# Kernel tuning notes

Measured on AMD Instinct MI355X. Metric: run time of the kernel, lower is better.

Reference implementation:

```python
import jax, jax.numpy as jnp
import numpy as np

B, T, V, E, H, DE = 64, 52, 10000, 512, 512, 2048


def _lstm_cell(x, h, c, w_ih, w_hh, b_ih, b_hh):
    # torch.nn.LSTMCell gate order: i, f, g, o
    gates = x @ w_ih.T + h @ w_hh.T + b_ih + b_hh
    i, f, g, o = jnp.split(gates, 4, axis=-1)
    c2 = jax.nn.sigmoid(f) * c + jax.nn.sigmoid(i) * jnp.tanh(g)
    h2 = jax.nn.sigmoid(o) * jnp.tanh(c2)
    return h2, c2


def _run_dir(emb_seq, img, lens, p1, p2, fc_w, fc_b):
    # emb_seq: [B, Td, E]; img: [B, H]; lens: [B] sorted descending.
    # The torch loop slices h[:batch_size_t]; since lens is sorted descending,
    # that is equivalent to masking updates where t >= (len-1). Rows that fall
    # out of the active prefix are never read again, and their predictions stay 0.
    Bd, Td = emb_seq.shape[0], emb_seq.shape[1]
    Hd = img.shape[1]
    mask = jnp.arange(Td)[None, :] < (lens - 1)[:, None]  # [B, Td]
    z = jnp.zeros((Bd, Hd), emb_seq.dtype)

    def step(carry, xs):
        h, c, h1, c1 = carry
        x, m = xs
        m2 = m[:, None]
        hn, cn = _lstm_cell(x, h, c, *p1)
        h1n, c1n = _lstm_cell(jnp.concatenate([hn, img], axis=1), h1, c1, *p2)
        carry = (jnp.where(m2, hn, h), jnp.where(m2, cn, c),
                 jnp.where(m2, h1n, h1), jnp.where(m2, c1n, c1))
        preds = jnp.where(m2, h1n @ fc_w.T + fc_b, 0.0)  # [B, V]
        return carry, preds

    _, preds = jax.lax.scan(step, (z, z, z, z), (emb_seq.transpose(1, 0, 2), mask.T))
    return preds.transpose(1, 0, 2)  # [B, Td, V]


def setup_inputs():
    key = jax.random.key(0)
    ks = iter(jax.random.split(key, 48))

    def u(shape, a=-0.1, b=0.1):
        return jax.random.uniform(next(ks), shape, minval=a, maxval=b, dtype=jnp.float32)

    inp = {}
    inp['encoder_out'] = jax.random.normal(next(ks), (B, DE), dtype=jnp.float32)
    inp['encoded_captions'] = jax.random.randint(next(ks), (B, T), 0, V)
    cl = jax.random.randint(next(ks), (B, 1), 2, T + 1)
    inp['caption_lengths'] = cl.at[0, 0].set(T)  # ensure max decode length = T-1
    # embeddings (uniform -0.1..0.1 per init_weights)
    inp['emb_w'] = u((V, E))
    inp['emb_r_w'] = u((V, E))
    # LSTM cells: torch default init uniform(-1/sqrt(H), 1/sqrt(H))
    kH = 1.0 / np.sqrt(H)
    for name, din in [('1', E), ('2', 2 * H), ('r1', E), ('r2', 2 * H)]:
        inp['w_ih' + name] = u((4 * H, din), -kH, kH)
        inp['w_hh' + name] = u((4 * H, H), -kH, kH)
        inp['b_ih' + name] = u((4 * H,), -kH, kH)
        inp['b_hh' + name] = u((4 * H,), -kH, kH)
    kD = 1.0 / np.sqrt(DE)
    inp['img_f_w'] = u((H, DE), -kD, kD)
    inp['img_f_b'] = u((H,), -kD, kD)
    inp['img_b_w'] = u((H, DE), -kD, kD)
    inp['img_b_b'] = u((H,), -kD, kD)
    inp['fc_w'] = u((V, H))
    inp['fc_b'] = jnp.zeros((V,), jnp.float32)
    inp['fcr_w'] = u((V, H))
    inp['fcr_b'] = jnp.zeros((V,), jnp.float32)
    return inp


def reference(encoder_out, encoded_captions, caption_lengths, emb_w, emb_r_w,
              w_ih1, w_hh1, b_ih1, b_hh1, w_ih2, w_hh2, b_ih2, b_hh2,
              w_ihr1, w_hhr1, b_ihr1, b_hhr1, w_ihr2, w_hhr2, b_ihr2, b_hhr2,
              img_f_w, img_f_b, img_b_w, img_b_b, fc_w, fc_b, fcr_w, fcr_b):
    lens = caption_lengths[:, 0]
    order = jnp.argsort(-lens)  # descending, stable (jax argsort is stable)
    lens = lens[order]
    enc = encoder_out[order]
    caps = encoded_captions[order]
    Tc = caps.shape[1]
    # per-row reversal of the first len tokens; rest zero (matches torch loop)
    j = jnp.arange(Tc)[None, :]
    valid = j < lens[:, None]
    rev_idx = jnp.where(valid, lens[:, None] - 1 - j, 0)
    caps_rev = jnp.where(valid, jnp.take_along_axis(caps, rev_idx, axis=1), 0)
    emb = emb_w[caps]          # [B, T, E]
    emb_r = emb_r_w[caps_rev]  # [B, T, E]
    img_f = enc @ img_f_w.T + img_f_b
    img_r = enc @ img_b_w.T + img_b_b
    Td = Tc - 1  # max(decode_lengths); setup guarantees max(lens) == T
    preds = _run_dir(emb[:, :Td], img_f, lens,
                     (w_ih1, w_hh1, b_ih1, b_hh1), (w_ih2, w_hh2, b_ih2, b_hh2), fc_w, fc_b)
    preds_r = _run_dir(emb_r[:, :Td], img_r, lens,
                       (w_ihr1, w_hhr1, b_ihr1, b_hhr1), (w_ihr2, w_hhr2, b_ihr2, b_hhr2), fcr_w, fcr_b)
    return preds, preds_r, caps, caps_rev, lens - 1, order
```

## Files before the change

### kernel.cpp

```cpp
#include <hip/hip_runtime.h>
#include <stdint.h>

#define B64   64
#define T52   52
#define TD    51
#define V10K  10000
#define MP    3328
#define MR    3264
#define NPFC  10112

typedef float  f32x4  __attribute__((ext_vector_type(4)));
typedef __bf16 bf16x8 __attribute__((ext_vector_type(8)));
typedef unsigned int u32x4 __attribute__((ext_vector_type(4)));
typedef unsigned short ushort_t;

__device__ inline unsigned short f2bf(float f) {
  unsigned u = __builtin_bit_cast(unsigned, f);
  u += 0x7fffu + ((u >> 16) & 1u);
  return (unsigned short)(u >> 16);
}
__device__ inline unsigned pack2(float a, float b) {
  return (unsigned)f2bf(a) | ((unsigned)f2bf(b) << 16);
}
__device__ inline float sigm(float x) { return 1.f / (1.f + expf(-x)); }

__device__ inline void store2_sc(ushort_t* p, unsigned v) {
  asm volatile("global_store_short %0, %1, off sc1" :: "v"(p), "v"(v) : "memory");
}
__device__ inline void loadA16(const ushort_t* a, u32x4 (&h)[16]) {
  asm volatile(
    "global_load_dwordx4 %0,  %16, off sc1\n\t"
    "global_load_dwordx4 %1,  %16, off offset:64 sc1\n\t"
    "global_load_dwordx4 %2,  %16, off offset:128 sc1\n\t"
    "global_load_dwordx4 %3,  %16, off offset:192 sc1\n\t"
    "global_load_dwordx4 %4,  %16, off offset:256 sc1\n\t"
    "global_load_dwordx4 %5,  %16, off offset:320 sc1\n\t"
    "global_load_dwordx4 %6,  %16, off offset:384 sc1\n\t"
    "global_load_dwordx4 %7,  %16, off offset:448 sc1\n\t"
    "global_load_dwordx4 %8,  %16, off offset:512 sc1\n\t"
    "global_load_dwordx4 %9,  %16, off offset:576 sc1\n\t"
    "global_load_dwordx4 %10, %16, off offset:640 sc1\n\t"
    "global_load_dwordx4 %11, %16, off offset:704 sc1\n\t"
    "global_load_dwordx4 %12, %16, off offset:768 sc1\n\t"
    "global_load_dwordx4 %13, %16, off offset:832 sc1\n\t"
    "global_load_dwordx4 %14, %16, off offset:896 sc1\n\t"
    "global_load_dwordx4 %15, %16, off offset:960 sc1\n\t"
    "s_waitcnt vmcnt(0)"
    : "=&v"(h[0]),"=&v"(h[1]),"=&v"(h[2]),"=&v"(h[3]),
      "=&v"(h[4]),"=&v"(h[5]),"=&v"(h[6]),"=&v"(h[7]),
      "=&v"(h[8]),"=&v"(h[9]),"=&v"(h[10]),"=&v"(h[11]),
      "=&v"(h[12]),"=&v"(h[13]),"=&v"(h[14]),"=&v"(h[15])
    : "v"(a) : "memory");
}
__device__ inline void loadA32(const ushort_t* a, const ushort_t* b,
                               u32x4 (&ha)[16], u32x4 (&hb)[16]) {
  asm volatile(
    "global_load_dwordx4 %0,  %32, off sc1\n\t"
    "global_load_dwordx4 %1,  %32, off offset:64 sc1\n\t"
    "global_load_dwordx4 %2,  %32, off offset:128 sc1\n\t"
    "global_load_dwordx4 %3,  %32, off offset:192 sc1\n\t"
    "global_load_dwordx4 %4,  %32, off offset:256 sc1\n\t"
    "global_load_dwordx4 %5,  %32, off offset:320 sc1\n\t"
    "global_load_dwordx4 %6,  %32, off offset:384 sc1\n\t"
    "global_load_dwordx4 %7,  %32, off offset:448 sc1\n\t"
    "global_load_dwordx4 %8,  %32, off offset:512 sc1\n\t"
    "global_load_dwordx4 %9,  %32, off offset:576 sc1\n\t"
    "global_load_dwordx4 %10, %32, off offset:640 sc1\n\t"
    "global_load_dwordx4 %11, %32, off offset:704 sc1\n\t"
    "global_load_dwordx4 %12, %32, off offset:768 sc1\n\t"
    "global_load_dwordx4 %13, %32, off offset:832 sc1\n\t"
    "global_load_dwordx4 %14, %32, off offset:896 sc1\n\t"
    "global_load_dwordx4 %15, %32, off offset:960 sc1\n\t"
    "global_load_dwordx4 %16, %33, off sc1\n\t"
    "global_load_dwordx4 %17, %33, off offset:64 sc1\n\t"
    "global_load_dwordx4 %18, %33, off offset:128 sc1\n\t"
    "global_load_dwordx4 %19, %33, off offset:192 sc1\n\t"
    "global_load_dwordx4 %20, %33, off offset:256 sc1\n\t"
    "global_load_dwordx4 %21, %33, off offset:320 sc1\n\t"
    "global_load_dwordx4 %22, %33, off offset:384 sc1\n\t"
    "global_load_dwordx4 %23, %33, off offset:448 sc1\n\t"
    "global_load_dwordx4 %24, %33, off offset:512 sc1\n\t"
    "global_load_dwordx4 %25, %33, off offset:576 sc1\n\t"
    "global_load_dwordx4 %26, %33, off offset:640 sc1\n\t"
    "global_load_dwordx4 %27, %33, off offset:704 sc1\n\t"
    "global_load_dwordx4 %28, %33, off offset:768 sc1\n\t"
    "global_load_dwordx4 %29, %33, off offset:832 sc1\n\t"
    "global_load_dwordx4 %30, %33, off offset:896 sc1\n\t"
    "global_load_dwordx4 %31, %33, off offset:960 sc1\n\t"
    "s_waitcnt vmcnt(0)"
    : "=&v"(ha[0]),"=&v"(ha[1]),"=&v"(ha[2]),"=&v"(ha[3]),
      "=&v"(ha[4]),"=&v"(ha[5]),"=&v"(ha[6]),"=&v"(ha[7]),
      "=&v"(ha[8]),"=&v"(ha[9]),"=&v"(ha[10]),"=&v"(ha[11]),
      "=&v"(ha[12]),"=&v"(ha[13]),"=&v"(ha[14]),"=&v"(ha[15]),
      "=&v"(hb[0]),"=&v"(hb[1]),"=&v"(hb[2]),"=&v"(hb[3]),
      "=&v"(hb[4]),"=&v"(hb[5]),"=&v"(hb[6]),"=&v"(hb[7]),
      "=&v"(hb[8]),"=&v"(hb[9]),"=&v"(hb[10]),"=&v"(hb[11]),
      "=&v"(hb[12]),"=&v"(hb[13]),"=&v"(hb[14]),"=&v"(hb[15])
    : "v"(a), "v"(b) : "memory");
}

__global__ void k_prep(const int* __restrict__ cl, const int* __restrict__ caps,
                       float* __restrict__ out_caps, float* __restrict__ out_capr,
                       float* __restrict__ out_lm1, float* __restrict__ out_ord,
                       int* __restrict__ order_i, int* __restrict__ lensm1_i,
                       int* __restrict__ nvtab, int* __restrict__ capsS,
                       int* __restrict__ capsRev)
{
  __shared__ int L[64], O[64], Ls_s[64];
  int i = threadIdx.x;
  L[i] = cl[i];
  __syncthreads();
  if (i == 0) {
    for (int a = 0; a < 64; ++a) O[a] = a;
    for (int a = 1; a < 64; ++a) {
      int key = O[a], kl = L[key], b = a - 1;
      while (b >= 0 && L[O[b]] < kl) { O[b + 1] = O[b]; --b; }
      O[b + 1] = key;
    }
  }
  __syncthreads();
  int src = O[i];
  int Ls  = L[src];
  Ls_s[i] = Ls;
  order_i[i]  = src;
  lensm1_i[i] = Ls - 1;
  out_lm1[i]  = (float)(Ls - 1);
  out_ord[i]  = (float)src;
  int rowLocal[T52];
  for (int t = 0; t < T52; ++t) {
    int c = caps[src * T52 + t];
    rowLocal[t] = c;
    capsS[i * T52 + t]    = c;
    out_caps[i * T52 + t] = (float)c;
  }
  for (int j = 0; j < T52; ++j) {
    int rv = (j < Ls) ? rowLocal[Ls - 1 - j] : 0;
    capsRev[i * T52 + j]  = rv;
    out_capr[i * T52 + j] = (float)rv;
  }
  __syncthreads();
  if (i < TD) {
    int nv = 0;
    for (int r = 0; r < 64; ++r) nv += (Ls_s[r] - 1 > i) ? 1 : 0;
    nvtab[i] = nv;
  }
}

__global__ void k_convert(const float* __restrict__ w_ih1, const float* __restrict__ w_ihr1,
                          const float* __restrict__ fc_w, const float* __restrict__ fcr_w,
                          const float* __restrict__ b_ih1, const float* __restrict__ b_hh1,
                          const float* __restrict__ b_ihr1, const float* __restrict__ b_hhr1,
                          const float* __restrict__ w_hh1, const float* __restrict__ w_hhr1,
                          const float* __restrict__ w_ih2, const float* __restrict__ w_ihr2,
                          const float* __restrict__ w_hh2, const float* __restrict__ w_hhr2,
                          const float* __restrict__ img_f_w, const float* __restrict__ img_b_w,
                          const float* __restrict__ b_ih2, const float* __restrict__ b_hh2,
                          const float* __restrict__ b_ihr2, const float* __restrict__ b_hhr2,
                          const float* __restrict__ enc, const int* __restrict__ order_i,
                          ushort_t* __restrict__ wih1bf, ushort_t* __restrict__ fcwbf,
                          ushort_t* __restrict__ whh1bf, ushort_t* __restrict__ wih2Lbf,
                          ushort_t* __restrict__ whh2bf, ushort_t* __restrict__ wih2Ibf,
                          ushort_t* __restrict__ imgwbf, ushort_t* __restrict__ encbf,
                          float* __restrict__ biasg1, float* __restrict__ biasg2)
{
  long long gid = (long long)blockIdx.x * blockDim.x + threadIdx.x;
  const long long C1 = 2048LL * 512 / 8;
  const long long CF = (long long)NPFC * 512 / 8;
  const long long bs  = 2 * C1 + 2 * CF;
  const long long bs2 = bs + 6 * C1;
  const long long bs3 = bs2 + 2 * C1;
  const long long bs4 = bs3 + 2 * C1;
  const long long bs5 = bs4 + 32768;
  if (gid < 2 * C1) {
    int dir = gid >= C1; long long cid = gid - (long long)dir * C1;
    const float* s = (dir ? w_ihr1 : w_ih1) + cid * 8;
    ushort_t* d = wih1bf + (long long)dir * 2048 * 512 + cid * 8;
    uint4 v;
    v.x = pack2(s[0], s[1]); v.y = pack2(s[2], s[3]);
    v.z = pack2(s[4], s[5]); v.w = pack2(s[6], s[7]);
    *(uint4*)d = v;
  } else if (gid < bs) {
    long long g2 = gid - 2 * C1; int dir = g2 >= CF;
    long long cid = g2 - (long long)dir * CF;
    long long row = cid >> 6; int k8 = (int)(cid & 63) * 8;
    ushort_t* d = fcwbf + (long long)dir * NPFC * 512 + row * 512 + k8;
    uint4 v;
    if (row < V10K) {
      const float* s = (dir ? fcr_w : fc_w) + row * 512 + k8;
      v.x = pack2(s[0], s[1]); v.y = pack2(s[2], s[3]);
      v.z = pack2(s[4], s[5]); v.w = pack2(s[6], s[7]);
    } else { v.x = v.y = v.z = v.w = 0u; }
    *(uint4*)d = v;
  } else if (gid < bs2) {
    long long e = gid - bs;
    int arr = (int)(e / (2 * C1));
    long long d2 = e - (long long)arr * 2 * C1;
    int dir = d2 >= C1;
    long long cid = d2 - (long long)dir * C1;
    long long row = cid >> 6; int k8 = (int)(cid & 63) * 8;
    const float* s;
    ushort_t* d;
    if (arr == 0)      { s = (dir ? w_hhr1 : w_hh1) + row * 512  + k8; d = whh1bf; }
    else if (arr == 1) { s = (dir ? w_ihr2 : w_ih2) + row * 1024 + k8; d = wih2Lbf; }
    else               { s = (dir ? w_hhr2 : w_hh2) + row * 512  + k8; d = whh2bf; }
    d += (long long)dir * 2048 * 512 + cid * 8;
    uint4 v;
    v.x = pack2(s[0], s[1]); v.y = pack2(s[2], s[3]);
    v.z = pack2(s[4], s[5]); v.w = pack2(s[6], s[7]);
    *(uint4*)d = v;
  } else if (gid < bs3) {
    long long e = gid - bs2; int dir = e >= C1;
    long long cid = e - (long long)dir * C1;
    long long row = cid >> 6; int k8 = (int)(cid & 63) * 8;
    const float* s = (dir ? w_ihr2 : w_ih2) + row * 1024 + 512 + k8;
    ushort_t* d = wih2Ibf + (long long)dir * 2048 * 512 + cid * 8;
    uint4 v;
    v.x = pack2(s[0], s[1]); v.y = pack2(s[2], s[3]);
    v.z = pack2(s[4], s[5]); v.w = pack2(s[6], s[7]);
    *(uint4*)d = v;
  } else if (gid < bs4) {
    long long e = gid - bs3; int dir = e >= C1;
    long long cid = e - (long long)dir * C1;
    long long row = cid >> 8; int c8 = (int)(cid & 255) * 8;
    const float* s = (dir ? img_b_w : img_f_w) + row * 2048 + c8;
    ushort_t* d = imgwbf + (long long)dir * 512 * 2048 + cid * 8;
    uint4 v;
    v.x = pack2(s[0], s[1]); v.y = pack2(s[2], s[3]);
    v.z = pack2(s[4], s[5]); v.w = pack2(s[6], s[7]);
    *(uint4*)d = v;
  } else if (gid < bs5) {
    long long cid = gid - bs4;
    int m = (int)(cid >> 8); int c8 = (int)(cid & 255) * 8;
    const float* s = enc + (long long)order_i[m & 63] * 2048 + c8;
    ushort_t* d = encbf + cid * 8;
    uint4 v;
    v.x = pack2(s[0], s[1]); v.y = pack2(s[2], s[3]);
    v.z = pack2(s[4], s[5]); v.w = pack2(s[6], s[7]);
    *(uint4*)d = v;
  } else {
    long long g3 = gid - bs5;
    if (g3 < 4096) {
      int dir = g3 >= 2048; int j = (int)(g3 & 2047);
      biasg1[dir * 2048 + j] = dir ? (b_ihr1[j] + b_hhr1[j]) : (b_ih1[j] + b_hh1[j]);
    } else if (g3 < 8192) {
      long long g4 = g3 - 4096;
      int dir = g4 >= 2048; int j = (int)(g4 & 2047);
      biasg2[dir * 2048 + j] = dir ? (b_ihr2[j] + b_hhr2[j]) : (b_ih2[j] + b_hh2[j]);
    }
  }
}

__global__ void k_gather(const float* __restrict__ emb_w, const float* __restrict__ emb_r_w,
                         const int* __restrict__ capsS, const int* __restrict__ capsRev,
                         ushort_t* __restrict__ embA)
{
  long long gid = (long long)blockIdx.x * 256 + threadIdx.x;
  const long long CPD = (long long)MP * 512 / 8;
  if (gid >= 2 * CPD) return;
  int dir = gid >= CPD; long long cid = gid - (long long)dir * CPD;
  int m = (int)(cid >> 6); int k8 = (int)(cid & 63) * 8;
  ushort_t* d = embA + (long long)dir * MP * 512 + (long long)m * 512 + k8;
  uint4 v;
  if (m < MR) {
    int b = m / TD, t = m - b * TD;
    int row = dir ? capsRev[b * T52 + t] : capsS[b * T52 + t];
    const float* s = (dir ? emb_r_w : emb_w) + (long long)row * 512 + k8;
    v.x = pack2(s[0], s[1]); v.y = pack2(s[2], s[3]);
    v.z = pack2(s[4], s[5]); v.w = pack2(s[6], s[7]);
  } else { v.x = v.y = v.z = v.w = 0u; }
  *(uint4*)d = v;
}

template<int MODE>
__global__ __launch_bounds__(256)
void k_gemm(const ushort_t* __restrict__ A0, long long As,
            const ushort_t* __restrict__ B0, long long Bs,
            const float* __restrict__ bias0, const float* __restrict__ bias1,
            void* __restrict__ out0, long long Os,
            const int* __restrict__ lensm1, int Nreal, int K)
{
  __shared__ ushort_t Ab[128 * 32];
  __shared__ ushort_t Bb[128 * 32];
  int dirz = blockIdx.z;
  const ushort_t* A = A0 + dirz * As;
  const ushort_t* Bm = B0 + dirz * Bs;
  const float* bias = dirz ? bias1 : bias0;
  int tid = threadIdx.x;
  int lane = tid & 63, wid = tid >> 6;
  int wr = wid >> 1, wc = wid & 1;
  long long tm = (long long)blockIdx.x * 128, tn = (long long)blockIdx.y * 128;
  f32x4 acc[4][4] = {};
  int c0 = tid, c1 = tid + 256;
  const ushort_t* Ag0 = A + (tm + (c0 >> 2)) * K + (c0 & 3) * 8;
  const ushort_t* Ag1 = A + (tm + (c1 >> 2)) * K + (c1 & 3) * 8;
  const ushort_t* Bg0 = Bm + (tn + (c0 >> 2)) * K + (c0 & 3) * 8;
  const ushort_t* Bg1 = Bm + (tn + (c1 >> 2)) * K + (c1 & 3) * 8;
  int KK = K >> 5;
  for (int kk = 0; kk < KK; ++kk) {
    uint4 va0 = *(const uint4*)(Ag0 + kk * 32);
    uint4 va1 = *(const uint4*)(Ag1 + kk * 32);
    uint4 vb0 = *(const uint4*)(Bg0 + kk * 32);
    uint4 vb1 = *(const uint4*)(Bg1 + kk * 32);
    __syncthreads();
    *(uint4*)&Ab[c0 * 8] = va0;
    *(uint4*)&Ab[c1 * 8] = va1;
    *(uint4*)&Bb[c0 * 8] = vb0;
    *(uint4*)&Bb[c1 * 8] = vb1;
    __syncthreads();
    int koff = (lane >> 4) * 8;
    bf16x8 av[4], bv[4];
    #pragma unroll
    for (int mi = 0; mi < 4; ++mi)
      av[mi] = *(const bf16x8*)&Ab[(wr * 64 + mi * 16 + (lane & 15)) * 32 + koff];
    #pragma unroll
    for (int ni = 0; ni < 4; ++ni)
      bv[ni] = *(const bf16x8*)&Bb[(wc * 64 + ni * 16 + (lane & 15)) * 32 + koff];
    #pragma unroll
    for (int mi = 0; mi < 4; ++mi)
      #pragma unroll
      for (int ni = 0; ni < 4; ++ni)
        acc[mi][ni] = __builtin_amdgcn_mfma_f32_16x16x32_bf16(av[mi], bv[ni], acc[mi][ni], 0, 0, 0);
  }
  #pragma unroll
  for (int mi = 0; mi < 4; ++mi) {
    #pragma unroll
    for (int rr = 0; rr < 4; ++rr) {
      long long m = tm + wr * 64 + mi * 16 + ((lane >> 4) * 4) + rr;
      if (MODE == 0) {
        float* orow = (float*)out0 + dirz * Os + m * (long long)Nreal;
        #pragma unroll
        for (int ni = 0; ni < 4; ++ni) {
          int n = (int)tn + wc * 64 + ni * 16 + (lane & 15);
          orow[n] = acc[mi][ni][rr] + bias[n];
        }
      } else if (MODE == 1) {
        if (m < MR) {
          int bb = (int)(m / TD); int tt = (int)(m - (long long)bb * TD);
          bool valid = tt < lensm1[bb];
          float* orow = (float*)out0 + dirz * Os + m * (long long)Nreal;
          #pragma unroll
          for (int ni = 0; ni < 4; ++ni) {
            int n = (int)tn + wc * 64 + ni * 16 + (lane & 15);
            if (n < Nreal) orow[n] = valid ? (acc[mi][ni][rr] + bias[n]) : 0.f;
          }
        }
      } else if (MODE == 2) {
        float bm = bias[m];
        float* orow = (float*)out0 + dirz * Os + m * (long long)Nreal;
        #pragma unroll
        for (int ni = 0; ni < 4; ++ni) {
          int n = (int)tn + wc * 64 + ni * 16 + (lane & 15);
          if (n < Nreal) orow[n] = acc[mi][ni][rr] + bm;
        }
      } else {
        ushort_t* orow = (ushort_t*)out0 + dirz * Os + m * (long long)Nreal;
        #pragma unroll
        for (int ni = 0; ni < 4; ++ni) {
          int n = (int)tn + wc * 64 + ni * 16 + (lane & 15);
          orow[n] = f2bf(acc[mi][ni][rr] + bias[n]);
        }
      }
    }
  }
}

__global__ __launch_bounds__(256)
void k_txg(const float* __restrict__ xg1, float* __restrict__ xg1T)
{
  int t = blockIdx.x, jt = blockIdx.y, dir = blockIdx.z;
  __shared__ float LT[64][65];
  const float* src = xg1 + (long long)dir * MP * 2048;
  int jj = threadIdx.x & 63, br = threadIdx.x >> 6;
  for (int q = 0; q < 16; ++q) {
    int b = br * 16 + q;
    LT[b][jj] = src[((long long)b * TD + t) * 2048 + jt * 64 + jj];
  }
  __syncthreads();
  float* dst = xg1T + (((long long)dir * TD + t) * 2048 + (long long)jt * 64) * 64;
  int j = threadIdx.x >> 2, seg = threadIdx.x & 3;
  for (int q = 0; q < 4; ++q) {
    int b0 = seg * 16 + q * 4;
    float4 v = { LT[b0][j], LT[b0 + 1][j], LT[b0 + 2][j], LT[b0 + 3][j] };
    *(float4*)(dst + (long long)j * 64 + b0) = v;
  }
}

__global__ __launch_bounds__(256, 1)
void k_rec(const ushort_t* __restrict__ whh1bf, const ushort_t* __restrict__ wih2Lbf,
           const ushort_t* __restrict__ whh2bf, const float* __restrict__ xg1T,
           const float* __restrict__ xg2imgT,
           ushort_t* __restrict__ h1hist,
           ushort_t* __restrict__ h2buf,
           ushort_t* __restrict__ h2allbf, const int* __restrict__ nvtab,
           int* __restrict__ slots)
{
  const int bid = blockIdx.x;
  const bool isL2 = bid >= 64;
  int dir, ht, half;
  if (!isL2) { dir = bid >> 5; ht = bid & 31; half = 0; }
  else { int idx = bid - 64; dir = idx >> 6; int sub = idx & 63; half = sub >> 5; ht = sub & 31; }
  const int tid = threadIdx.x;
  const int lane = tid & 63, mt = tid >> 6;
  const int l15 = lane & 15, l4 = lane >> 4;
  const int jl = ht * 16 + l15;

  __shared__ ushort_t Wl[32768];
  __shared__ ushort_t Wi[32768];
  __shared__ int nv_s[64];

  {
    const ushort_t* src = (isL2 ? whh2bf : whh1bf) + (long long)dir * 2048 * 512;
    #pragma unroll
    for (int i = 0; i < 16; ++i) {
      int c = tid + i * 256;
      int nl = c >> 6;
      int kb = (c & 63) * 16;
      int row = (nl >> 4) * 512 + ht * 16 + (nl & 15);
      u32x4 v = *(const u32x4*)(src + (long long)row * 512 + (long long)(c & 63) * 8);
      *(u32x4*)((char*)Wl + nl * 1024 + (kb ^ ((nl & 7) << 4))) = v;
    }
    if (isL2) {
      const ushort_t* src2 = wih2Lbf + (long long)dir * 2048 * 512;
      #pragma unroll
      for (int i = 0; i < 16; ++i) {
        int c = tid + i * 256;
        int nl = c >> 6;
        int kb = (c & 63) * 16;
        int row = (nl >> 4) * 512 + ht * 16 + (nl & 15);
        u32x4 v = *(const u32x4*)(src2 + (long long)row * 512 + (long long)(c & 63) * 8);
        *(u32x4*)((char*)Wi + nl * 1024 + (kb ^ ((nl & 7) << 4))) = v;
      }
    }
    if (tid < TD) nv_s[tid] = nvtab[tid];
  }
  __syncthreads();

  int* aS = slots + dir * 32;
  int* bS = slots + 64 + dir * 64;

  if (!isL2) {
    const int r0 = mt * 16 + l4 * 4;
    f32x4 creg = {0.f, 0.f, 0.f, 0.f};
    for (int t = 0; t < TD; ++t) {
      bool act = (mt * 16 < nv_s[t]);
      f32x4 xv[4];
      if (act) {
        const float* xg = xg1T + ((long long)dir * TD + t) * (2048 * 64);
        #pragma unroll
        for (int g = 0; g < 4; ++g)
          xv[g] = *(const f32x4*)(xg + (long long)(g * 512 + jl) * 64 + r0);
      }
      if (t > 0) {
        if (mt == 0) {
          for (;;) {
            int v = __hip_atomic_load(&aS[lane & 31], __ATOMIC_RELAXED, __HIP_MEMORY_SCOPE_AGENT);
            if (__all(v >= t)) break;
          }
        }
        __syncthreads();
      }
      if (act) {
        const ushort_t* hsrc = h1hist + ((long long)t * 2 + dir) * (64 * 512);
        u32x4 hv[16];
        loadA16(hsrc + (long long)(mt * 16 + l15) * 512 + l4 * 8, hv);
        f32x4 acc[4] = {};
        #pragma unroll
        for (int kk = 0; kk < 16; ++kk) {
          bf16x8 av = __builtin_bit_cast(bf16x8, hv[kk]);
          int kb = kk * 64 + l4 * 16;
          #pragma unroll
          for (int g = 0; g < 4; ++g) {
            bf16x8 bv = *(const bf16x8*)((const char*)Wl + (g * 16 + l15) * 1024 + (kb ^ ((l15 & 7) << 4)));
            acc[g] = __builtin_amdgcn_mfma_f32_16x16x32_bf16(av, bv, acc[g], 0, 0, 0);
          }
        }
        ushort_t* hdst = h1hist + ((long long)(t + 1) * 2 + dir) * (64 * 512);
        f32x4 cn;
        #pragma unroll
        for (int rr = 0; rr < 4; ++rr) {
          float gi = acc[0][rr] + xv[0][rr];
          float gf = acc[1][rr] + xv[1][rr];
          float gg = acc[2][rr] + xv[2][rr];
          float go = acc[3][rr] + xv[3][rr];
          float c = sigm(gf) * creg[rr] + sigm(gi) * tanhf(gg);
          float h = sigm(go) * tanhf(c);
          cn[rr] = c;
          store2_sc(hdst + (long long)(r0 + rr) * 512 + jl, (unsigned)f2bf(h));
        }
        creg = cn;
      }
      __syncthreads();
      if (tid == 0)
        __hip_atomic_store(&aS[ht], t + 1, __ATOMIC_RELAXED, __HIP_MEMORY_SCOPE_AGENT);
    }
  } else {
    const int r0 = half * 32 + mt * 16 + l4 * 4;
    f32x4 xv2[4];
    {
      const float* xg = xg2imgT + (long long)dir * (2048 * 64);
      #pragma unroll
      for (int g = 0; g < 4; ++g)
        xv2[g] = *(const f32x4*)(xg + (long long)(g * 512 + jl) * 64 + (half * 32 + (mt & 1) * 16 + l4 * 4));
    }
    f32x4 creg = {0.f, 0.f, 0.f, 0.f};
    for (int t = 0; t < TD; ++t) {
      if (mt == 0) {
        for (;;) {
          int va = __hip_atomic_load(&aS[lane & 31], __ATOMIC_RELAXED, __HIP_MEMORY_SCOPE_AGENT);
          int vb = __hip_atomic_load(&bS[lane], __ATOMIC_RELAXED, __HIP_MEMORY_SCOPE_AGENT);
          if (__all((va >= t + 1) & (vb >= t))) break;
        }
      }
      __syncthreads();
      int nv = nv_s[t];
      if (mt < 2 && half * 32 + mt * 16 < nv) {
        const ushort_t* h1s = h1hist + ((long long)(t + 1) * 2 + dir) * (64 * 512);
        const ushort_t* h2s = h2buf + ((long long)((t + 1) & 1) * 2 + dir) * (64 * 512);
        u32x4 ha[16], hb[16];
        loadA32(h1s + (long long)(half * 32 + mt * 16 + l15) * 512 + l4 * 8,
                h2s + (long long)(half * 32 + mt * 16 + l15) * 512 + l4 * 8, ha, hb);
        f32x4 acc[4] = {};
        #pragma unroll
        for (int kk = 0; kk < 16; ++kk) {
          bf16x8 av = __builtin_bit_cast(bf16x8, ha[kk]);
          int kb = kk * 64 + l4 * 16;
          #pragma unroll
          for (int g = 0; g < 4; ++g) {
            bf16x8 bv = *(const bf16x8*)((const char*)Wi + (g * 16 + l15) * 1024 + (kb ^ ((l15 & 7) << 4)));
            acc[g] = __builtin_amdgcn_mfma_f32_16x16x32_bf16(av, bv, acc[g], 0, 0, 0);
          }
        }
        #pragma unroll
        for (int kk = 0; kk < 16; ++kk) {
          bf16x8 av = __builtin_bit_cast(bf16x8, hb[kk]);
          int kb = kk * 64 + l4 * 16;
          #pragma unroll
          for (int g = 0; g < 4; ++g) {
            bf16x8 bv = *(const bf16x8*)((const char*)Wl + (g * 16 + l15) * 1024 + (kb ^ ((l15 & 7) << 4)));
            acc[g] = __builtin_amdgcn_mfma_f32_16x16x32_bf16(av, bv, acc[g], 0, 0, 0);
          }
        }
        ushort_t* h2n = h2buf + ((long long)(t & 1) * 2 + dir) * (64 * 512);
        ushort_t* h2a = h2allbf + (long long)dir * MP * 512;
        f32x4 cn;
        #pragma unroll
        for (int rr = 0; rr < 4; ++rr) {
          float gi = acc[0][rr] + xv2[0][rr];
          float gf = acc[1][rr] + xv2[1][rr];
          float gg = acc[2][rr] + xv2[2][rr];
          float go = acc[3][rr] + xv2[3][rr];
          float c = sigm(gf) * creg[rr] + sigm(gi) * tanhf(gg);
          float h = sigm(go) * tanhf(c);
          cn[rr] = c;
          ushort_t hbb = f2bf(h);
          store2_sc(h2n + (long long)(r0 + rr) * 512 + jl, (unsigned)hbb);
          if (r0 + rr < nv)
            h2a[((long long)(r0 + rr) * TD + t) * 512 + jl] = hbb;
        }
        creg = cn;
      }
      __syncthreads();
      if (tid == 0)
        __hip_atomic_store(&bS[half * 32 + ht], t + 1, __ATOMIC_RELAXED, __HIP_MEMORY_SCOPE_AGENT);
    }
  }
}

extern "C" void kernel_launch(void* const* d_in, const int* in_sizes, int n_in,
                              void* d_out, int out_size, void* d_ws, size_t ws_size,
                              hipStream_t stream)
{
  const float* enc     = (const float*)d_in[0];
  const int*   caps    = (const int*)d_in[1];
  const int*   cl      = (const int*)d_in[2];
  const float* emb_w   = (const float*)d_in[3];
  const float* emb_r_w = (const float*)d_in[4];
  const float* w_ih1   = (const float*)d_in[5];
  const float* w_hh1   = (const float*)d_in[6];
  const float* b_ih1   = (const float*)d_in[7];
  const float* b_hh1   = (const float*)d_in[8];
  const float* w_ih2   = (const float*)d_in[9];
  const float* w_hh2   = (const float*)d_in[10];
  const float* b_ih2   = (const float*)d_in[11];
  const float* b_hh2   = (const float*)d_in[12];
  const float* w_ihr1  = (const float*)d_in[13];
  const float* w_hhr1  = (const float*)d_in[14];
  const float* b_ihr1  = (const float*)d_in[15];
  const float* b_hhr1  = (const float*)d_in[16];
  const float* w_ihr2  = (const float*)d_in[17];
  const float* w_hhr2  = (const float*)d_in[18];
  const float* b_ihr2  = (const float*)d_in[19];
  const float* b_hhr2  = (const float*)d_in[20];
  const float* img_f_w = (const float*)d_in[21];
  const float* img_f_b = (const float*)d_in[22];
  const float* img_b_w = (const float*)d_in[23];
  const float* img_b_b = (const float*)d_in[24];
  const float* fc_w    = (const float*)d_in[25];
  const float* fc_b    = (const float*)d_in[26];
  const float* fcr_w   = (const float*)d_in[27];
  const float* fcr_b   = (const float*)d_in[28];

  float* outF = (float*)d_out;
  const long long PRED = (long long)MR * V10K;
  float* o_caps = outF + 2 * PRED;
  float* o_capr = o_caps + B64 * T52;
  float* o_lm1  = o_capr + B64 * T52;
  float* o_ord  = o_lm1 + B64;
  float*    xg1       = outF;
  float*    xg1T      = outF + 14000000;
  ushort_t* whh1bf    = (ushort_t*)(outF + 27500000);
  ushort_t* wih2Lbf   = (ushort_t*)(outF + 28600000);
  ushort_t* whh2bf    = (ushort_t*)(outF + 29700000);
  ushort_t* h1hist    = (ushort_t*)(outF + 31000000);
  ushort_t* wih2Ibf   = (ushort_t*)(outF + 34600000);
  ushort_t* imgwbf    = (ushort_t*)(outF + 35700000);
  ushort_t* encbf     = (ushort_t*)(outF + 36800000);
  ushort_t* imgbf     = (ushort_t*)(outF + 37000000);

  char* w = (char*)d_ws;
  auto alloc = [&](size_t bytes) -> char* {
    char* p = w; w += (bytes + 255) & ~(size_t)255; return p;
  };
  int*      order_i  = (int*)alloc(64 * 4);
  int*      lensm1_i = (int*)alloc(64 * 4);
  int*      nvtab    = (int*)alloc(64 * 4);
  int*      capsS    = (int*)alloc(B64 * T52 * 4);
  int*      capsRev  = (int*)alloc(B64 * T52 * 4);
  float*    biasg1   = (float*)alloc(2 * 2048 * 4);
  float*    biasg2   = (float*)alloc(2 * 2048 * 4);
  float*    xg2imgT  = (float*)alloc((size_t)2 * 2048 * 64 * 4);
  char*     stateBase = alloc(262144 + 1024);
  ushort_t* h2buf = (ushort_t*)stateBase;
  int*      slotp = (int*)(stateBase + 262144);
  ushort_t* embA    = (ushort_t*)alloc((size_t)2 * MP * 512 * 2);
  ushort_t* wih1bf  = (ushort_t*)alloc((size_t)2 * 2048 * 512 * 2);
  ushort_t* fcwbf   = (ushort_t*)alloc((size_t)2 * NPFC * 512 * 2);
  ushort_t* h2allbf = (ushort_t*)alloc((size_t)2 * MP * 512 * 2);

  hipMemsetAsync(stateBase, 0, 262144 + 1024, stream);
  hipMemsetAsync(h1hist, 0, 131072, stream);

  k_prep<<<1, 64, 0, stream>>>(cl, caps, o_caps, o_capr, o_lm1, o_ord,
                               order_i, lensm1_i, nvtab, capsS, capsRev);
  k_convert<<<11360, 256, 0, stream>>>(w_ih1, w_ihr1, fc_w, fcr_w,
                                       b_ih1, b_hh1, b_ihr1, b_hhr1,
                                       w_hh1, w_hhr1, w_ih2, w_ihr2, w_hh2, w_hhr2,
                                       img_f_w, img_b_w, b_ih2, b_hh2, b_ihr2, b_hhr2,
                                       enc, order_i,
                                       wih1bf, fcwbf, whh1bf, wih2Lbf, whh2bf,
                                       wih2Ibf, imgwbf, encbf, biasg1, biasg2);
  k_gather<<<1664, 256, 0, stream>>>(emb_w, emb_r_w, capsS, capsRev, embA);
  k_gemm<3><<<dim3(1, 4, 2), 256, 0, stream>>>(encbf, 0LL,
                                               imgwbf, 512LL * 2048,
                                               img_f_b, img_b_b,
                                               imgbf, 128LL * 512,
                                               nullptr, 512, 2048);
  k_gemm<2><<<dim3(16, 1, 2), 256, 0, stream>>>(wih2Ibf, 2048LL * 512,
                                                imgbf, 128LL * 512,
                                                biasg2, biasg2 + 2048,
                                                xg2imgT, 2048LL * 64,
                                                nullptr, 64, 512);
  k_gemm<0><<<dim3(26, 16, 2), 256, 0, stream>>>(embA, (long long)MP * 512,
                                                 wih1bf, 2048LL * 512,
                                                 biasg1, biasg1 + 2048,
                                                 xg1, (long long)MP * 2048,
                                                 nullptr, 2048, 512);
  k_txg<<<dim3(TD, 32, 2), 256, 0, stream>>>(xg1, xg1T);
  k_rec<<<192, 256, 0, stream>>>(whh1bf, wih2Lbf, whh2bf, xg1T, xg2imgT,
                                 h1hist, h2buf, h2allbf, nvtab, slotp);
  k_gemm<1><<<dim3(26, 79, 2), 256, 0, stream>>>(h2allbf, (long long)MP * 512,
                                                 fcwbf, (long long)NPFC * 512,
                                                 fc_b, fcr_b,
                                                 outF, PRED,
                                                 lensm1_i, V10K, 512);
}
```

Baseline: 810.6 us.

## Compact valid rows for FC GEMM and drop xg1 transpose kernel

```diff
diff --git a/kernel.cpp b/kernel.cpp
--- a/kernel.cpp
+++ b/kernel.cpp
@@ -104,9 +104,11 @@
                        float* __restrict__ out_lm1, float* __restrict__ out_ord,
                        int* __restrict__ order_i, int* __restrict__ lensm1_i,
                        int* __restrict__ nvtab, int* __restrict__ capsS,
-                       int* __restrict__ capsRev)
+                       int* __restrict__ capsRev, int* __restrict__ cumtab,
+                       int* __restrict__ rowmap)
 {
-  __shared__ int L[64], O[64], Ls_s[64];
+  __shared__ int L[64], O[64], Ls_s[64], Cum[65];
+  __shared__ int C_s[64][T52];
   int i = threadIdx.x;
   L[i] = cl[i];
   __syncthreads();
@@ -126,19 +128,27 @@
   lensm1_i[i] = Ls - 1;
   out_lm1[i]  = (float)(Ls - 1);
   out_ord[i]  = (float)src;
-  int rowLocal[T52];
   for (int t = 0; t < T52; ++t) {
     int c = caps[src * T52 + t];
-    rowLocal[t] = c;
+    C_s[i][t] = c;
     capsS[i * T52 + t]    = c;
     out_caps[i * T52 + t] = (float)c;
   }
+  __syncthreads();
   for (int j = 0; j < T52; ++j) {
-    int rv = (j < Ls) ? rowLocal[Ls - 1 - j] : 0;
+    int rv = (j < Ls) ? C_s[i][Ls - 1 - j] : 0;
     capsRev[i * T52 + j]  = rv;
     out_capr[i * T52 + j] = (float)rv;
   }
+  if (i == 0) {
+    int s = 0;
+    for (int b = 0; b < 64; ++b) { Cum[b] = s; s += Ls_s[b] - 1; }
+    Cum[64] = s;
+  }
   __syncthreads();
+  cumtab[i] = Cum[i];
+  if (i == 0) cumtab[64] = Cum[64];
+  for (int t = 0; t < Ls - 1; ++t) rowmap[Cum[i] + t] = i * TD + t;
   if (i < TD) {
     int nv = 0;
     for (int r = 0; r < 64; ++r) nv += (Ls_s[r] - 1 > i) ? 1 : 0;
@@ -277,7 +287,7 @@
             const ushort_t* __restrict__ B0, long long Bs,
             const float* __restrict__ bias0, const float* __restrict__ bias1,
             void* __restrict__ out0, long long Os,
-            const int* __restrict__ lensm1, int Nreal, int K)
+            int Nreal, int K)
 {
   __shared__ ushort_t Ab[128 * 32];
   __shared__ ushort_t Bb[128 * 32];
@@ -333,17 +343,6 @@
           int n = (int)tn + wc * 64 + ni * 16 + (lane & 15);
           orow[n] = acc[mi][ni][rr] + bias[n];
         }
-      } else if (MODE == 1) {
-        if (m < MR) {
-          int bb = (int)(m / TD); int tt = (int)(m - (long long)bb * TD);
-          bool valid = tt < lensm1[bb];
-          float* orow = (float*)out0 + dirz * Os + m * (long long)Nreal;
-          #pragma unroll
-          for (int ni = 0; ni < 4; ++ni) {
-            int n = (int)tn + wc * 64 + ni * 16 + (lane & 15);
-            if (n < Nreal) orow[n] = valid ? (acc[mi][ni][rr] + bias[n]) : 0.f;
-          }
-        }
       } else if (MODE == 2) {
         float bm = bias[m];
         float* orow = (float*)out0 + dirz * Os + m * (long long)Nreal;
@@ -365,33 +364,99 @@
 }
 
 __global__ __launch_bounds__(256)
-void k_txg(const float* __restrict__ xg1, float* __restrict__ xg1T)
+void k_fc(const ushort_t* __restrict__ A0, const ushort_t* __restrict__ B0,
+          const float* __restrict__ bias0, const float* __restrict__ bias1,
+          float* __restrict__ out0, const int* __restrict__ rowmap,
+          const int* __restrict__ cumtab)
 {
-  int t = blockIdx.x, jt = blockIdx.y, dir = blockIdx.z;
-  __shared__ float LT[64][65];
-  const float* src = xg1 + (long long)dir * MP * 2048;
-  int jj = threadIdx.x & 63, br = threadIdx.x >> 6;
-  for (int q = 0; q < 16; ++q) {
-    int b = br * 16 + q;
-    LT[b][jj] = src[((long long)b * TD + t) * 2048 + jt * 64 + jj];
-  }
-  __syncthreads();
-  float* dst = xg1T + (((long long)dir * TD + t) * 2048 + (long long)jt * 64) * 64;
-  int j = threadIdx.x >> 2, seg = threadIdx.x & 3;
-  for (int q = 0; q < 4; ++q) {
-    int b0 = seg * 16 + q * 4;
-    float4 v = { LT[b0][j], LT[b0 + 1][j], LT[b0 + 2][j], LT[b0 + 3][j] };
-    *(float4*)(dst + (long long)j * 64 + b0) = v;
+  const long long PRED = (long long)MR * V10K;
+  int Mc = cumtab[64];
+  long long tm = (long long)blockIdx.x * 128;
+  if (tm >= Mc) return;
+  __shared__ ushort_t Ab[128 * 32];
+  __shared__ ushort_t Bb[128 * 32];
+  int dirz = blockIdx.z;
+  const ushort_t* A = A0 + (long long)dirz * MP * 512;
+  const ushort_t* Bm = B0 + (long long)dirz * NPFC * 512;
+  const float* bias = dirz ? bias1 : bias0;
+  float* out = out0 + (long long)dirz * PRED;
+  int tid = threadIdx.x;
+  int lane = tid & 63, wid = tid >> 6;
+  int wr = wid >> 1, wc = wid & 1;
+  long long tn = (long long)blockIdx.y * 128;
+  f32x4 acc[4][4] = {};
+  int c0 = tid, c1 = tid + 256;
+  const ushort_t* Ag0 = A + (tm + (c0 >> 2)) * 512 + (c0 & 3) * 8;
+  const ushort_t* Ag1 = A + (tm + (c1 >> 2)) * 512 + (c1 & 3) * 8;
+  const ushort_t* Bg0 = Bm + (tn + (c0 >> 2)) * 512 + (c0 & 3) * 8;
+  const ushort_t* Bg1 = Bm + (tn + (c1 >> 2)) * 512 + (c1 & 3) * 8;
+  for (int kk = 0; kk < 16; ++kk) {
+    uint4 va0 = *(const uint4*)(Ag0 + kk * 32);
+    uint4 va1 = *(const uint4*)(Ag1 + kk * 32);
+    uint4 vb0 = *(const uint4*)(Bg0 + kk * 32);
+    uint4 vb1 = *(const uint4*)(Bg1 + kk * 32);
+    __syncthreads();
+    *(uint4*)&Ab[c0 * 8] = va0;
+    *(uint4*)&Ab[c1 * 8] = va1;
+    *(uint4*)&Bb[c0 * 8] = vb0;
+    *(uint4*)&Bb[c1 * 8] = vb1;
+    __syncthreads();
+    int koff = (lane >> 4) * 8;
+    bf16x8 av[4], bv[4];
+    #pragma unroll
+    for (int mi = 0; mi < 4; ++mi)
+      av[mi] = *(const bf16x8*)&Ab[(wr * 64 + mi * 16 + (lane & 15)) * 32 + koff];
+    #pragma unroll
+    for (int ni = 0; ni < 4; ++ni)
+      bv[ni] = *(const bf16x8*)&Bb[(wc * 64 + ni * 16 + (lane & 15)) * 32 + koff];
+    #pragma unroll
+    for (int mi = 0; mi < 4; ++mi)
+      #pragma unroll
+      for (int ni = 0; ni < 4; ++ni)
+        acc[mi][ni] = __builtin_amdgcn_mfma_f32_16x16x32_bf16(av[mi], bv[ni], acc[mi][ni], 0, 0, 0);
+  }
+  #pragma unroll
+  for (int mi = 0; mi < 4; ++mi) {
+    #pragma unroll
+    for (int rr = 0; rr < 4; ++rr) {
+      long long c = tm + wr * 64 + mi * 16 + ((lane >> 4) * 4) + rr;
+      if (c < Mc) {
+        int m = rowmap[c];
+        float* orow = out + (long long)m * V10K;
+        #pragma unroll
+        for (int ni = 0; ni < 4; ++ni) {
+          int n = (int)tn + wc * 64 + ni * 16 + (lane & 15);
+          if (n < V10K) orow[n] = acc[mi][ni][rr] + bias[n];
+        }
+      }
+    }
+  }
+}
+
+__global__ __launch_bounds__(256)
+void k_zero(float* __restrict__ outF, const int* __restrict__ lensm1_i)
+{
+  const long long PRED = (long long)MR * V10K;
+  int m = blockIdx.x;
+  int b = m / TD, t = m - b * TD;
+  if (t < lensm1_i[b]) return;
+  float4 z = {0.f, 0.f, 0.f, 0.f};
+  float* r0 = outF + (long long)m * V10K;
+  float* r1 = outF + PRED + (long long)m * V10K;
+  for (int i = threadIdx.x; i < 2500; i += 256) {
+    ((float4*)r0)[i] = z;
+    ((float4*)r1)[i] = z;
   }
 }
 
 __global__ __launch_bounds__(256, 1)
 void k_rec(const ushort_t* __restrict__ whh1bf, const ushort_t* __restrict__ wih2Lbf,
-           const ushort_t* __restrict__ whh2bf, const float* __restrict__ xg1T,
+           const ushort_t* __restrict__ whh2bf, const float* __restrict__ xg1,
            const float* __restrict__ xg2imgT,
            ushort_t* __restrict__ h1hist,
            ushort_t* __restrict__ h2buf,
-           ushort_t* __restrict__ h2allbf, const int* __restrict__ nvtab,
+           ushort_t* __restrict__ h2allbf,
+           const int* __restrict__ nvtab, const int* __restrict__ cumtab,
            int* __restrict__ slots)
 {
   const int bid = blockIdx.x;
@@ -407,6 +472,7 @@
   __shared__ ushort_t Wl[32768];
   __shared__ ushort_t Wi[32768];
   __shared__ int nv_s[64];
+  __shared__ int cum_s[64];
 
   {
     const ushort_t* src = (isL2 ? whh2bf : whh1bf) + (long long)dir * 2048 * 512;
@@ -432,6 +498,7 @@
       }
     }
     if (tid < TD) nv_s[tid] = nvtab[tid];
+    if (tid < 64) cum_s[tid] = cumtab[tid];
   }
   __syncthreads();
 
@@ -443,12 +510,15 @@
     f32x4 creg = {0.f, 0.f, 0.f, 0.f};
     for (int t = 0; t < TD; ++t) {
       bool act = (mt * 16 < nv_s[t]);
-      f32x4 xv[4];
+      float xs[4][4];
       if (act) {
-        const float* xg = xg1T + ((long long)dir * TD + t) * (2048 * 64);
-        #pragma unroll
-        for (int g = 0; g < 4; ++g)
-          xv[g] = *(const f32x4*)(xg + (long long)(g * 512 + jl) * 64 + r0);
+        #pragma unroll
+        for (int rr = 0; rr < 4; ++rr) {
+          const float* xr = xg1 + ((long long)dir * MP + (long long)(r0 + rr) * TD + t) * 2048;
+          #pragma unroll
+          for (int g = 0; g < 4; ++g)
+            xs[g][rr] = xr[g * 512 + jl];
+        }
       }
       if (t > 0) {
         if (mt == 0) {
@@ -478,10 +548,10 @@
         f32x4 cn;
         #pragma unroll
         for (int rr = 0; rr < 4; ++rr) {
-          float gi = acc[0][rr] + xv[0][rr];
-          float gf = acc[1][rr] + xv[1][rr];
-          float gg = acc[2][rr] + xv[2][rr];
-          float go = acc[3][rr] + xv[3][rr];
+          float gi = acc[0][rr] + xs[0][rr];
+          float gf = acc[1][rr] + xs[1][rr];
+          float gg = acc[2][rr] + xs[2][rr];
+          float go = acc[3][rr] + xs[3][rr];
           float c = sigm(gf) * creg[rr] + sigm(gi) * tanhf(gg);
           float h = sigm(go) * tanhf(c);
           cn[rr] = c;
@@ -555,7 +625,7 @@
           ushort_t hbb = f2bf(h);
           store2_sc(h2n + (long long)(r0 + rr) * 512 + jl, (unsigned)hbb);
           if (r0 + rr < nv)
-            h2a[((long long)(r0 + rr) * TD + t) * 512 + jl] = hbb;
+            h2a[((long long)(cum_s[r0 + rr] + t)) * 512 + jl] = hbb;
         }
         creg = cn;
       }
@@ -607,7 +677,6 @@
   float* o_lm1  = o_capr + B64 * T52;
   float* o_ord  = o_lm1 + B64;
   float*    xg1       = outF;
-  float*    xg1T      = outF + 14000000;
   ushort_t* whh1bf    = (ushort_t*)(outF + 27500000);
   ushort_t* wih2Lbf   = (ushort_t*)(outF + 28600000);
   ushort_t* whh2bf    = (ushort_t*)(outF + 29700000);
@@ -624,6 +693,8 @@
   int*      order_i  = (int*)alloc(64 * 4);
   int*      lensm1_i = (int*)alloc(64 * 4);
   int*      nvtab    = (int*)alloc(64 * 4);
+  int*      cumtab   = (int*)alloc(65 * 4);
+  int*      rowmap   = (int*)alloc(MR * 4);
   int*      capsS    = (int*)alloc(B64 * T52 * 4);
   int*      capsRev  = (int*)alloc(B64 * T52 * 4);
   float*    biasg1   = (float*)alloc(2 * 2048 * 4);
@@ -641,7 +712,8 @@
   hipMemsetAsync(h1hist, 0, 131072, stream);
 
   k_prep<<<1, 64, 0, stream>>>(cl, caps, o_caps, o_capr, o_lm1, o_ord,
-                               order_i, lensm1_i, nvtab, capsS, capsRev);
+                               order_i, lensm1_i, nvtab, capsS, capsRev,
+                               cumtab, rowmap);
   k_convert<<<11360, 256, 0, stream>>>(w_ih1, w_ihr1, fc_w, fcr_w,
                                        b_ih1, b_hh1, b_ihr1, b_hhr1,
                                        w_hh1, w_hhr1, w_ih2, w_ihr2, w_hh2, w_hhr2,
@@ -654,23 +726,20 @@
                                                imgwbf, 512LL * 2048,
                                                img_f_b, img_b_b,
                                                imgbf, 128LL * 512,
-                                               nullptr, 512, 2048);
+                                               512, 2048);
   k_gemm<2><<<dim3(16, 1, 2), 256, 0, stream>>>(wih2Ibf, 2048LL * 512,
                                                 imgbf, 128LL * 512,
                                                 biasg2, biasg2 + 2048,
                                                 xg2imgT, 2048LL * 64,
-                                                nullptr, 64, 512);
+                                                64, 512);
   k_gemm<0><<<dim3(26, 16, 2), 256, 0, stream>>>(embA, (long long)MP * 512,
                                                  wih1bf, 2048LL * 512,
                                                  biasg1, biasg1 + 2048,
                                                  xg1, (long long)MP * 2048,
-                                                 nullptr, 2048, 512);
-  k_txg<<<dim3(TD, 32, 2), 256, 0, stream>>>(xg1, xg1T);
-  k_rec<<<192, 256, 0, stream>>>(whh1bf, wih2Lbf, whh2bf, xg1T, xg2imgT,
-                                 h1hist, h2buf, h2allbf, nvtab, slotp);
-  k_gemm<1><<<dim3(26, 79, 2), 256, 0, stream>>>(h2allbf, (long long)MP * 512,
-                                                 fcwbf, (long long)NPFC * 512,
-                                                 fc_b, fcr_b,
-                                                 outF, PRED,
-                                                 lensm1_i, V10K, 512);
-}
+                                                 2048, 512);
+  k_rec<<<192, 256, 0, stream>>>(whh1bf, wih2Lbf, whh2bf, xg1, xg2imgT,
+                                 h1hist, h2buf, h2allbf, nvtab, cumtab, slotp);
+  k_zero<<<MR, 256, 0, stream>>>(outF, lensm1_i);
+  k_fc<<<dim3(26, 79, 2), 256, 0, stream>>>(h2allbf, fcwbf, fc_b, fcr_b,
+                                            outF, rowmap, cumtab);
+}
```

Measured after the change: 752.0 us. 7.2% less time.
